# Kernel optimization log

Measured on AMD Instinct MI355X. Metric: run time of the kernel, lower is better.

Reference implementation:

```python
import jax, jax.numpy as jnp
import numpy as np
from jax.scipy.special import logsumexp

N, T, C, H, V = 8, 512, 1024, 256, 32000


def _res_layer(x, W1, b1, W2, b2):
    # hmm-lm ResLayer: x + ReLU(Linear(ReLU(Linear(x))))
    return x + jax.nn.relu(jax.nn.relu(x @ W1.T + b1) @ W2.T + b2)


def setup_inputs() -> dict:
    key = jax.random.key(0)
    ks = jax.random.split(key, 12)
    g = lambda k, shape: jax.random.normal(k, shape, jnp.float32) * (1.0 / np.sqrt(shape[-1]))
    return {
        "text": jax.random.randint(ks[0], (N, T), 0, V),
        "start_emb": jax.random.normal(ks[1], (H,), jnp.float32),
        "start_lin_W": g(ks[2], (H, H)),
        "start_lin_b": jnp.zeros((H,), jnp.float32),
        "start_res_W1": g(ks[3], (2, H, H)),
        "start_res_b1": jnp.zeros((2, H), jnp.float32),
        "start_res_W2": g(ks[4], (2, H, H)),
        "start_res_b2": jnp.zeros((2, H), jnp.float32),
        "state_emb": g(ks[5], (C, H)),
        "next_state_emb": g(ks[6], (C, H)),
        "preterminal_emb": g(ks[7], (C, H)),
        "term_res_W1": g(ks[8], (2, H, H)),
        "term_res_b1": jnp.zeros((2, H), jnp.float32),
        "term_res_W2": g(ks[9], (2, H, H)),
        "term_res_b2": jnp.zeros((2, H), jnp.float32),
        "terminal_emb": g(ks[10], (V, H)),
    }


def reference(text, start_emb, start_lin_W, start_lin_b,
              start_res_W1, start_res_b1, start_res_W2, start_res_b2,
              state_emb, next_state_emb, preterminal_emb,
              term_res_W1, term_res_b1, term_res_W2, term_res_b2,
              terminal_emb):
    # --- start distribution: start_mlp(start_emb) @ next_state_emb.T (tie_start) ---
    fx = start_emb @ start_lin_W.T + start_lin_b
    for i in range(2):
        fx = _res_layer(fx, start_res_W1[i], start_res_b1[i], start_res_W2[i], start_res_b2[i])
    start = jax.nn.log_softmax(fx @ next_state_emb.T)            # [C]

    # --- transition: log_softmax(state_emb @ next_state_emb.T) ---
    transition = jax.nn.log_softmax(state_emb @ next_state_emb.T, axis=-1)  # [C, C]

    # --- emission: log_softmax(terminal_mlp(preterminal_emb) @ terminal_emb.T) ---
    ft = preterminal_emb
    for i in range(2):
        ft = _res_layer(ft, term_res_W1[i], term_res_b1[i], term_res_W2[i], term_res_b2[i])
    emission = jax.nn.log_softmax(ft @ terminal_emb.T, axis=-1)  # [C, V]
    emis_t = emission.T                                          # [V, C]

    # --- HMM forward (log-space) scan; evidence = logsumexp(alpha_T) summed over batch ---
    alpha0 = start[None, :] + emis_t[text[:, 0]]                 # [N, C]

    def step(alpha, x_t):
        # alpha: [N, C]; x_t: [N]
        a = logsumexp(alpha[:, :, None] + transition[None], axis=1) + emis_t[x_t]
        return a, None

    alpha_T, _ = jax.lax.scan(step, alpha0, text[:, 1:].T)       # time-major [T-1, N]
    evidence = logsumexp(alpha_T, axis=-1).sum()
    return evidence
```

## Files before the change

### kernel.cpp

```cpp
#include <hip/hip_runtime.h>
#include <stdint.h>
#include <stddef.h>

#define N_ 8
#define T_ 512
#define C_ 1024
#define H_ 256
#define V_ 32000
#define KC 32
#define CW 32

#define OFF_START   0u
#define OFF_LSE     4096u
#define OFF_EVP     8192u
#define OFF_EA      16384u
#define OFF_FT      81920u
#define OFF_P       1130496u
#define OFF_PART    5324800u
#define OFF_EEXP    5849088u

typedef __attribute__((ext_vector_type(8))) short short8;
typedef __attribute__((ext_vector_type(4))) float floatx4;

__device__ __forceinline__ float dot4(float4 a, float4 b) {
  return a.x*b.x + a.y*b.y + a.z*b.z + a.w*b.w;
}

__device__ __forceinline__ unsigned short f2bf(float f) {
  unsigned u = __float_as_uint(f);
  unsigned r = u + 0x7fffu + ((u >> 16) & 1u);
  return (unsigned short)(r >> 16);
}

__device__ __forceinline__ unsigned pk_bf2(float x, float y) {
  return ((unsigned)f2bf(y) << 16) | (unsigned)f2bf(x);
}

__device__ __forceinline__ short8 pack8(float4 a, float4 b) {
  union { short8 s; unsigned u[4]; } r;
  r.u[0] = pk_bf2(a.x, a.y);
  r.u[1] = pk_bf2(a.z, a.w);
  r.u[2] = pk_bf2(b.x, b.y);
  r.u[3] = pk_bf2(b.z, b.w);
  return r.s;
}

__global__ __launch_bounds__(256) void k_start(
    const float* __restrict__ se, const float* __restrict__ lw, const float* __restrict__ lb,
    const float* __restrict__ W1, const float* __restrict__ b1,
    const float* __restrict__ W2, const float* __restrict__ b2,
    const float* __restrict__ nse, float* __restrict__ out_start)
{
  __shared__ float xs[H_], fx[H_], h1[H_];
  __shared__ float lg[C_];
  __shared__ float redk[4];
  int tid = threadIdx.x;
  xs[tid] = se[tid];
  __syncthreads();
  {
    float acc = lb[tid];
    const float4* wr = (const float4*)(lw + (size_t)tid*H_);
    for (int k = 0; k < H_/4; ++k) acc += dot4(wr[k], *(const float4*)&xs[k*4]);
    fx[tid] = acc;
  }
  __syncthreads();
  for (int L = 0; L < 2; ++L) {
    {
      float acc = b1[L*H_ + tid];
      const float4* wr = (const float4*)(W1 + (size_t)(L*H_ + tid)*H_);
      for (int k = 0; k < H_/4; ++k) acc += dot4(wr[k], *(const float4*)&fx[k*4]);
      h1[tid] = fmaxf(acc, 0.f);
    }
    __syncthreads();
    {
      float acc = b2[L*H_ + tid];
      const float4* wr = (const float4*)(W2 + (size_t)(L*H_ + tid)*H_);
      for (int k = 0; k < H_/4; ++k) acc += dot4(wr[k], *(const float4*)&h1[k*4]);
      fx[tid] += fmaxf(acc, 0.f);
    }
    __syncthreads();
  }
  float lmax = -1e30f;
  for (int r = 0; r < 4; ++r) {
    int cc = tid + r*256;
    float acc = 0.f;
    const float4* er = (const float4*)(nse + (size_t)cc*H_);
    for (int k = 0; k < H_/4; ++k) acc += dot4(er[k], *(const float4*)&fx[k*4]);
    lg[cc] = acc;
    lmax = fmaxf(lmax, acc);
  }
  for (int m = 32; m; m >>= 1) lmax = fmaxf(lmax, __shfl_xor(lmax, m, 64));
  if ((tid & 63) == 0) redk[tid >> 6] = lmax;
  __syncthreads();
  float M = fmaxf(fmaxf(redk[0], redk[1]), fmaxf(redk[2], redk[3]));
  __syncthreads();
  float ssum = 0.f;
  for (int r = 0; r < 4; ++r) ssum += __expf(lg[tid + r*256] - M);
  for (int m = 32; m; m >>= 1) ssum += __shfl_xor(ssum, m, 64);
  if ((tid & 63) == 0) redk[tid >> 6] = ssum;
  __syncthreads();
  float S = redk[0] + redk[1] + redk[2] + redk[3];
  float lse = M + __logf(S);
  for (int r = 0; r < 4; ++r) {
    int cc = tid + r*256;
    out_start[cc] = lg[cc] - lse;
  }
}

__global__ __launch_bounds__(256) void k_gemm_cc(
    const float* __restrict__ A, const float* __restrict__ B, float* __restrict__ Cout)
{
  __shared__ float As[64][69];
  __shared__ float Bs[64][69];
  int tid = threadIdx.x;
  int bi = blockIdx.y, bj = blockIdx.x;
  int sr = tid >> 2, sq = tid & 3;
  int tx = tid & 15, ty = tid >> 4;
  float acc[4][4] = {};
  for (int kb = 0; kb < H_; kb += 64) {
    __syncthreads();
    {
      const float* ar = A + (size_t)(bi*64 + sr)*H_ + kb + sq*16;
      const float* br = B + (size_t)(bj*64 + sr)*H_ + kb + sq*16;
#pragma unroll
      for (int qq = 0; qq < 4; ++qq) {
        float4 av = *(const float4*)(ar + qq*4);
        float4 bv = *(const float4*)(br + qq*4);
        int kk = sq*16 + qq*4;
        As[sr][kk+0]=av.x; As[sr][kk+1]=av.y; As[sr][kk+2]=av.z; As[sr][kk+3]=av.w;
        Bs[sr][kk+0]=bv.x; Bs[sr][kk+1]=bv.y; Bs[sr][kk+2]=bv.z; Bs[sr][kk+3]=bv.w;
      }
    }
    __syncthreads();
#pragma unroll 4
    for (int k = 0; k < 64; ++k) {
      float a0 = As[ty*4+0][k], a1 = As[ty*4+1][k], a2 = As[ty*4+2][k], a3 = As[ty*4+3][k];
      float b0 = Bs[tx*4+0][k], b1 = Bs[tx*4+1][k], b2 = Bs[tx*4+2][k], b3 = Bs[tx*4+3][k];
      acc[0][0]+=a0*b0; acc[0][1]+=a0*b1; acc[0][2]+=a0*b2; acc[0][3]+=a0*b3;
      acc[1][0]+=a1*b0; acc[1][1]+=a1*b1; acc[1][2]+=a1*b2; acc[1][3]+=a1*b3;
      acc[2][0]+=a2*b0; acc[2][1]+=a2*b1; acc[2][2]+=a2*b2; acc[2][3]+=a2*b3;
      acc[3][0]+=a3*b0; acc[3][1]+=a3*b1; acc[3][2]+=a3*b2; acc[3][3]+=a3*b3;
    }
  }
#pragma unroll
  for (int ii = 0; ii < 4; ++ii)
#pragma unroll
    for (int jj = 0; jj < 4; ++jj)
      Cout[(size_t)(bi*64 + ty*4 + ii)*C_ + bj*64 + tx*4 + jj] = acc[ii][jj];
}

__global__ __launch_bounds__(256) void k_softmax_rows(float* __restrict__ P)
{
  __shared__ float redk[4];
  int row = blockIdx.x, tid = threadIdx.x;
  float4* pr = (float4*)(P + (size_t)row*C_);
  float4 v = pr[tid];
  float m = fmaxf(fmaxf(v.x, v.y), fmaxf(v.z, v.w));
  for (int mm = 32; mm; mm >>= 1) m = fmaxf(m, __shfl_xor(m, mm, 64));
  if ((tid & 63) == 0) redk[tid >> 6] = m;
  __syncthreads();
  float M = fmaxf(fmaxf(redk[0], redk[1]), fmaxf(redk[2], redk[3]));
  __syncthreads();
  float4 e;
  e.x = __expf(v.x - M); e.y = __expf(v.y - M); e.z = __expf(v.z - M); e.w = __expf(v.w - M);
  float s = e.x + e.y + e.z + e.w;
  for (int mm = 32; mm; mm >>= 1) s += __shfl_xor(s, mm, 64);
  if ((tid & 63) == 0) redk[tid >> 6] = s;
  __syncthreads();
  float S = redk[0] + redk[1] + redk[2] + redk[3];
  float inv = 1.0f / S;
  e.x *= inv; e.y *= inv; e.z *= inv; e.w *= inv;
  pr[tid] = e;
}

__global__ __launch_bounds__(256) void k_mlp(
    const float* __restrict__ inp, const float* __restrict__ W1, const float* __restrict__ b1,
    const float* __restrict__ W2, const float* __restrict__ b2, float* __restrict__ ft)
{
  __shared__ float xs[4][H_];
  __shared__ float hs[4][H_];
  int tid = threadIdx.x;
  int r0 = blockIdx.x * 4;
  int lr = tid >> 6, lc = (tid & 63) * 4;
  *(float4*)&xs[lr][lc] = *(const float4*)(inp + (size_t)(r0+lr)*H_ + lc);
  __syncthreads();
  for (int L = 0; L < 2; ++L) {
    {
      const float4* wr = (const float4*)(W1 + (size_t)(L*H_ + tid)*H_);
      float bb = b1[L*H_ + tid];
      float a0=bb, a1=bb, a2=bb, a3=bb;
      for (int k = 0; k < H_/4; ++k) {
        float4 w = wr[k];
        a0 += dot4(w, *(const float4*)&xs[0][k*4]);
        a1 += dot4(w, *(const float4*)&xs[1][k*4]);
        a2 += dot4(w, *(const float4*)&xs[2][k*4]);
        a3 += dot4(w, *(const float4*)&xs[3][k*4]);
      }
      hs[0][tid]=fmaxf(a0,0.f); hs[1][tid]=fmaxf(a1,0.f);
      hs[2][tid]=fmaxf(a2,0.f); hs[3][tid]=fmaxf(a3,0.f);
    }
    __syncthreads();
    {
      const float4* wr = (const float4*)(W2 + (size_t)(L*H_ + tid)*H_);
      float bb = b2[L*H_ + tid];
      float a0=bb, a1=bb, a2=bb, a3=bb;
      for (int k = 0; k < H_/4; ++k) {
        float4 w = wr[k];
        a0 += dot4(w, *(const float4*)&hs[0][k*4]);
        a1 += dot4(w, *(const float4*)&hs[1][k*4]);
        a2 += dot4(w, *(const float4*)&hs[2][k*4]);
        a3 += dot4(w, *(const float4*)&hs[3][k*4]);
      }
      xs[0][tid] += fmaxf(a0,0.f); xs[1][tid] += fmaxf(a1,0.f);
      xs[2][tid] += fmaxf(a2,0.f); xs[3][tid] += fmaxf(a3,0.f);
    }
    __syncthreads();
  }
  *(float4*)(ft + (size_t)(r0+lr)*H_ + lc) = *(float4*)&xs[lr][lc];
}

#define LSE_VSPLIT 16
#define LSE_VPB    2000
#define LSE_CHUNKS 125

__global__ __launch_bounds__(256) void k_lse_mfma(
    const float* __restrict__ ft, const float* __restrict__ emb, float* __restrict__ part)
{
  int tid = threadIdx.x;
  int lane = tid & 63;
  int w = tid >> 6;
  int q = blockIdx.x;
  int jb = blockIdx.y * 64 + w * 16;
  int r16 = lane & 15, kb = lane >> 4;

  short8 A[8];
  {
    const float* arow = ft + (size_t)(jb + r16) * H_ + kb * 8;
#pragma unroll
    for (int ks = 0; ks < 8; ++ks) {
      float4 a = *(const float4*)(arow + ks * 32);
      float4 b = *(const float4*)(arow + ks * 32 + 4);
      A[ks] = pack8(a, b);
    }
  }
  float s0 = 0.f, s1 = 0.f, s2 = 0.f, s3 = 0.f;
  const float* embq = emb + (size_t)q * LSE_VPB * H_;
#pragma unroll 1
  for (int ch = 0; ch < LSE_CHUNKS; ++ch) {
    const float* brow = embq + (size_t)(ch * 16 + r16) * H_ + kb * 8;
    floatx4 acca = {0,0,0,0}, accb = {0,0,0,0};
#pragma unroll
    for (int ks = 0; ks < 8; ks += 2) {
      float4 x0 = *(const float4*)(brow + ks * 32);
      float4 y0 = *(const float4*)(brow + ks * 32 + 4);
      float4 x1 = *(const float4*)(brow + ks * 32 + 32);
      float4 y1 = *(const float4*)(brow + ks * 32 + 36);
      acca = __builtin_amdgcn_mfma_f32_16x16x32_bf16(A[ks],   pack8(x0, y0), acca, 0, 0, 0);
      accb = __builtin_amdgcn_mfma_f32_16x16x32_bf16(A[ks+1], pack8(x1, y1), accb, 0, 0, 0);
    }
    s0 += __expf(acca[0] + accb[0]);
    s1 += __expf(acca[1] + accb[1]);
    s2 += __expf(acca[2] + accb[2]);
    s3 += __expf(acca[3] + accb[3]);
  }
#pragma unroll
  for (int mm = 1; mm <= 8; mm <<= 1) {
    s0 += __shfl_xor(s0, mm, 64);
    s1 += __shfl_xor(s1, mm, 64);
    s2 += __shfl_xor(s2, mm, 64);
    s3 += __shfl_xor(s3, mm, 64);
  }
  if (r16 == 0) {
    int jrow = jb + kb * 4;
    part[(size_t)(jrow + 0) * LSE_VSPLIT + q] = s0;
    part[(size_t)(jrow + 1) * LSE_VSPLIT + q] = s1;
    part[(size_t)(jrow + 2) * LSE_VSPLIT + q] = s2;
    part[(size_t)(jrow + 3) * LSE_VSPLIT + q] = s3;
  }
}

__global__ __launch_bounds__(256) void k_lse_reduce(
    const float* __restrict__ part, float* __restrict__ lse_row)
{
  int row = blockIdx.x * 256 + threadIdx.x;
  const float4* p = (const float4*)(part + (size_t)row * LSE_VSPLIT);
  float4 a = p[0], b = p[1], c = p[2], d = p[3];
  float s = a.x+a.y+a.z+a.w + b.x+b.y+b.z+b.w + c.x+c.y+c.z+c.w + d.x+d.y+d.z+d.w;
  lse_row[row] = __logf(s);
}

__global__ __launch_bounds__(256) void k_eexp_mfma(
    const float* __restrict__ ft, const float* __restrict__ emb, const int* __restrict__ text,
    const float* __restrict__ lse_row, float* __restrict__ EEXP)
{
  int tid = threadIdx.x;
  int lane = tid & 63;
  int w = tid >> 6;
  int jb = blockIdx.y * 64 + w * 16;
  int tb = blockIdx.x * 64;
  int r16 = lane & 15, kb = lane >> 4;

  short8 A[8];
  {
    const float* arow = ft + (size_t)(jb + r16) * H_ + kb * 8;
#pragma unroll
    for (int ks = 0; ks < 8; ++ks) {
      float4 a = *(const float4*)(arow + ks * 32);
      float4 b = *(const float4*)(arow + ks * 32 + 4);
      A[ks] = pack8(a, b);
    }
  }
  float4 lsej = *(const float4*)(lse_row + jb + kb * 4);

#pragma unroll 1
  for (int tc = 0; tc < 4; ++tc) {
    int idx = tb + tc * 16 + r16;
    int tok = text[idx];
    const float* brow = emb + (size_t)tok * H_ + kb * 8;
    floatx4 acca = {0,0,0,0}, accb = {0,0,0,0};
#pragma unroll
    for (int ks = 0; ks < 8; ks += 2) {
      float4 x0 = *(const float4*)(brow + ks * 32);
      float4 y0 = *(const float4*)(brow + ks * 32 + 4);
      float4 x1 = *(const float4*)(brow + ks * 32 + 32);
      float4 y1 = *(const float4*)(brow + ks * 32 + 36);
      acca = __builtin_amdgcn_mfma_f32_16x16x32_bf16(A[ks],   pack8(x0, y0), acca, 0, 0, 0);
      accb = __builtin_amdgcn_mfma_f32_16x16x32_bf16(A[ks+1], pack8(x1, y1), accb, 0, 0, 0);
    }
    float4 o;
    o.x = __expf(acca[0] + accb[0] - lsej.x);
    o.y = __expf(acca[1] + accb[1] - lsej.y);
    o.z = __expf(acca[2] + accb[2] - lsej.z);
    o.w = __expf(acca[3] + accb[3] - lsej.w);
    *(float4*)(EEXP + (size_t)idx * C_ + jb + kb * 4) = o;
  }
}

#define SCAN_LDS 75792

#define BF_ACC(PU, RI) { \
    float plo_ = __uint_as_float((PU) << 16); \
    float phi_ = __uint_as_float((PU) & 0xffff0000u); \
    acc[jo][0] += plo_ * ea0[(RI)];   acc[jo][0] += phi_ * ea0[(RI)+1]; \
    acc[jo][1] += plo_ * ea1[(RI)];   acc[jo][1] += phi_ * ea1[(RI)+1]; }

__global__ __launch_bounds__(256) void k_scan(
    const float* __restrict__ P, const float* __restrict__ EEXP, const float* __restrict__ startv,
    unsigned* __restrict__ eaG, float* __restrict__ evp)
{
  extern __shared__ char smem[];
  char*  Pl  = smem;
  float* eal = (float*)(smem + 65536);
  float* red = (float*)(smem + 65536 + 9216);
  float* gmw = (float*)(smem + 65536 + 9216 + 1024);

  int tid = threadIdx.x;
  int bid = blockIdx.x;
  int c  = bid >> 2;
  int ng = bid & 3;
  int n0 = ng * 2;

  if (tid < 64) {
    int nn = tid >> 5, j = tid & 31;
    int jj = c*CW + j;
    float val = __expf(startv[jj]) * EEXP[((size_t)(n0+nn)*T_ + 0)*C_ + jj];
    unsigned word = ((unsigned)f2bf(val) << 16) | 1u;
    __hip_atomic_store(&eaG[(size_t)(0*N_ + n0+nn)*C_ + jj], word,
                       __ATOMIC_RELAXED, __HIP_MEMORY_SCOPE_AGENT);
  }

  {
    int j4  = (tid & 7) * 4;
    int swz = (tid & 7) << 4;
    int irow = tid >> 3;
    for (int rep = 0; rep < 32; ++rep) {
      int i = rep*32 + irow;
      float4 v = *(const float4*)(P + (size_t)i*C_ + c*CW + j4);
      int ib = (i*2) ^ swz;
      *(unsigned short*)(Pl + (j4+0)*2048 + ib) = f2bf(v.x);
      *(unsigned short*)(Pl + (j4+1)*2048 + ib) = f2bf(v.y);
      *(unsigned short*)(Pl + (j4+2)*2048 + ib) = f2bf(v.z);
      *(unsigned short*)(Pl + (j4+3)*2048 + ib) = f2bf(v.w);
    }
  }
  __syncthreads();

  float logscale0 = 0.f, logscale1 = 0.f;

#pragma unroll 1
  for (int t = 1; t < T_; ++t) {
    int pprev = (t-1) & 1, pcur = t & 1;

    float eexp_reg = 0.f;
    if (tid < 64) {
      int nn = tid >> 5, j = tid & 31;
      eexp_reg = EEXP[((size_t)(n0+nn)*T_ + t)*C_ + c*CW + j];
    }

    {
      int seq = tid >> 7;
      int ib  = (tid & 127) * 8;
      unsigned long long* src = (unsigned long long*)(eaG + ((size_t)(pprev*N_ + n0+seq)*C_ + ib));
      unsigned tgt = (unsigned)t;
      unsigned long long v0, v1, v2, v3;
      int guard = 0;
      for (;;) {
        v0 = __hip_atomic_load(src+0, __ATOMIC_RELAXED, __HIP_MEMORY_SCOPE_AGENT);
        v1 = __hip_atomic_load(src+1, __ATOMIC_RELAXED, __HIP_MEMORY_SCOPE_AGENT);
        v2 = __hip_atomic_load(src+2, __ATOMIC_RELAXED, __HIP_MEMORY_SCOPE_AGENT);
        v3 = __hip_atomic_load(src+3, __ATOMIC_RELAXED, __HIP_MEMORY_SCOPE_AGENT);
        bool ok = (((unsigned)v0 & 0xffffu) == tgt) & (((unsigned)(v0>>32) & 0xffffu) == tgt)
                & (((unsigned)v1 & 0xffffu) == tgt) & (((unsigned)(v1>>32) & 0xffffu) == tgt)
                & (((unsigned)v2 & 0xffffu) == tgt) & (((unsigned)(v2>>32) & 0xffffu) == tgt)
                & (((unsigned)v3 & 0xffffu) == tgt) & (((unsigned)(v3>>32) & 0xffffu) == tgt);
        if (ok) break;
        __builtin_amdgcn_s_sleep(1);
        if (++guard > 2000000) break;
      }
      float f0 = __uint_as_float((unsigned)v0        & 0xffff0000u);
      float f1 = __uint_as_float((unsigned)(v0>>32)  & 0xffff0000u);
      float f2 = __uint_as_float((unsigned)v1        & 0xffff0000u);
      float f3 = __uint_as_float((unsigned)(v1>>32)  & 0xffff0000u);
      float f4v= __uint_as_float((unsigned)v2        & 0xffff0000u);
      float f5 = __uint_as_float((unsigned)(v2>>32)  & 0xffff0000u);
      float f6 = __uint_as_float((unsigned)v3        & 0xffff0000u);
      float f7 = __uint_as_float((unsigned)(v3>>32)  & 0xffff0000u);
      int idx = ib + ((ib >> 5) << 2);
      float* dst = &eal[seq*1152 + idx];
      dst[0]=f0; dst[1]=f1; dst[2]=f2; dst[3]=f3;
      dst[4]=f4v; dst[5]=f5; dst[6]=f6; dst[7]=f7;
      float m8 = fmaxf(fmaxf(fmaxf(f0,f1),fmaxf(f2,f3)), fmaxf(fmaxf(f4v,f5),fmaxf(f6,f7)));
#pragma unroll
      for (int mm = 32; mm; mm >>= 1) m8 = fmaxf(m8, __shfl_xor(m8, mm, 64));
      if ((tid & 63) == 0) gmw[tid >> 6] = m8;
    }
    __syncthreads();

    float M0 = fmaxf(gmw[0], gmw[1]);
    float M1 = fmaxf(gmw[2], gmw[3]);
    logscale0 += __logf(M0);
    logscale1 += __logf(M1);

    float ea0[32], ea1[32];
    {
      int s = tid >> 3;
      int eb = s * 36;
#pragma unroll
      for (int w = 0; w < 8; ++w) {
        float4 a = *(const float4*)&eal[eb + w*4];
        float4 b = *(const float4*)&eal[1152 + eb + w*4];
        ea0[w*4+0]=a.x; ea0[w*4+1]=a.y; ea0[w*4+2]=a.z; ea0[w*4+3]=a.w;
        ea1[w*4+0]=b.x; ea1[w*4+1]=b.y; ea1[w*4+2]=b.z; ea1[w*4+3]=b.w;
      }
    }
    float acc[4][2] = {{0,0},{0,0},{0,0},{0,0}};
    {
      int g = tid & 7, s = tid >> 3;
      int i0b = s * 64;
      int swz = g << 4;
#pragma unroll
      for (int jo = 0; jo < 4; ++jo) {
        const char* bp = Pl + (size_t)(g*4 + jo)*2048;
#pragma unroll
        for (int u = 0; u < 4; ++u) {
          uint4 pk = *(const uint4*)(bp + ((i0b + u*16) ^ swz));
          BF_ACC(pk.x, u*8+0)
          BF_ACC(pk.y, u*8+2)
          BF_ACC(pk.z, u*8+4)
          BF_ACC(pk.w, u*8+6)
        }
      }
    }
#pragma unroll
    for (int jo = 0; jo < 4; ++jo)
#pragma unroll
      for (int nn = 0; nn < 2; ++nn) {
        float vv = acc[jo][nn];
        vv += __shfl_xor(vv, 8, 64);
        vv += __shfl_xor(vv, 16, 64);
        vv += __shfl_xor(vv, 32, 64);
        acc[jo][nn] = vv;
      }
    if ((tid & 63) < 8) {
      int wv = tid >> 6, g = tid & 7;
#pragma unroll
      for (int jo = 0; jo < 4; ++jo) {
        red[((wv*8 + g)*4 + jo)*2 + 0] = acc[jo][0];
        red[((wv*8 + g)*4 + jo)*2 + 1] = acc[jo][1];
      }
    }
    __syncthreads();
    if (tid < 64) {
      int nn = tid >> 5, j = tid & 31;
      int gg = j >> 2, joo = j & 3;
      float sum = red[((0*8+gg)*4+joo)*2+nn] + red[((1*8+gg)*4+joo)*2+nn]
                + red[((2*8+gg)*4+joo)*2+nn] + red[((3*8+gg)*4+joo)*2+nn];
      float M = (nn == 0) ? M0 : M1;
      float val = (sum / M) * eexp_reg;
      unsigned word = ((unsigned)f2bf(val) << 16) | (unsigned)(t+1);
      __hip_atomic_store(&eaG[(size_t)(pcur*N_ + n0+nn)*C_ + c*CW + j], word,
                         __ATOMIC_RELAXED, __HIP_MEMORY_SCOPE_AGENT);
    }
  }

  if (c == 0) {
    {
      int seq = tid >> 7;
      int ib  = (tid & 127) * 8;
      unsigned long long* src = (unsigned long long*)(eaG + ((size_t)(1*N_ + n0+seq)*C_ + ib));
      unsigned tgt = (unsigned)T_;
      unsigned long long v0, v1, v2, v3;
      int guard = 0;
      for (;;) {
        v0 = __hip_atomic_load(src+0, __ATOMIC_RELAXED, __HIP_MEMORY_SCOPE_AGENT);
        v1 = __hip_atomic_load(src+1, __ATOMIC_RELAXED, __HIP_MEMORY_SCOPE_AGENT);
        v2 = __hip_atomic_load(src+2, __ATOMIC_RELAXED, __HIP_MEMORY_SCOPE_AGENT);
        v3 = __hip_atomic_load(src+3, __ATOMIC_RELAXED, __HIP_MEMORY_SCOPE_AGENT);
        bool ok = (((unsigned)v0 & 0xffffu) == tgt) & (((unsigned)(v0>>32) & 0xffffu) == tgt)
                & (((unsigned)v1 & 0xffffu) == tgt) & (((unsigned)(v1>>32) & 0xffffu) == tgt)
                & (((unsigned)v2 & 0xffffu) == tgt) & (((unsigned)(v2>>32) & 0xffffu) == tgt)
                & (((unsigned)v3 & 0xffffu) == tgt) & (((unsigned)(v3>>32) & 0xffffu) == tgt);
        if (ok) break;
        __builtin_amdgcn_s_sleep(1);
        if (++guard > 2000000) break;
      }
      float s8 = __uint_as_float((unsigned)v0       & 0xffff0000u)
               + __uint_as_float((unsigned)(v0>>32) & 0xffff0000u)
               + __uint_as_float((unsigned)v1       & 0xffff0000u)
               + __uint_as_float((unsigned)(v1>>32) & 0xffff0000u)
               + __uint_as_float((unsigned)v2       & 0xffff0000u)
               + __uint_as_float((unsigned)(v2>>32) & 0xffff0000u)
               + __uint_as_float((unsigned)v3       & 0xffff0000u)
               + __uint_as_float((unsigned)(v3>>32) & 0xffff0000u);
#pragma unroll
      for (int mm = 32; mm; mm >>= 1) s8 += __shfl_xor(s8, mm, 64);
      if ((tid & 63) == 0) gmw[tid >> 6] = s8;
    }
    __syncthreads();
    if (tid == 0) {
      float S0 = gmw[0] + gmw[1];
      float S1 = gmw[2] + gmw[3];
      evp[n0]     = logscale0 + __logf(S0);
      evp[n0 + 1] = logscale1 + __logf(S1);
    }
  }
}

__global__ void k_final(const float* __restrict__ evp, float* __restrict__ out)
{
  if (threadIdx.x == 0) {
    float s = 0.f;
#pragma unroll
    for (int i = 0; i < N_; ++i) s += evp[i];
    out[0] = s;
  }
}

extern "C" void kernel_launch(void* const* d_in, const int* in_sizes, int n_in,
                              void* d_out, int out_size, void* d_ws, size_t ws_size,
                              hipStream_t stream)
{
  const int*   text      = (const int*)  d_in[0];
  const float* start_emb = (const float*)d_in[1];
  const float* slw       = (const float*)d_in[2];
  const float* slb       = (const float*)d_in[3];
  const float* sW1       = (const float*)d_in[4];
  const float* sb1       = (const float*)d_in[5];
  const float* sW2       = (const float*)d_in[6];
  const float* sb2       = (const float*)d_in[7];
  const float* state_emb = (const float*)d_in[8];
  const float* nse       = (const float*)d_in[9];
  const float* pre_emb   = (const float*)d_in[10];
  const float* tW1       = (const float*)d_in[11];
  const float* tb1       = (const float*)d_in[12];
  const float* tW2       = (const float*)d_in[13];
  const float* tb2       = (const float*)d_in[14];
  const float* term_emb  = (const float*)d_in[15];

  char* ws = (char*)d_ws;
  float*    w_start = (float*)   (ws + OFF_START);
  float*    w_lse   = (float*)   (ws + OFF_LSE);
  float*    w_evp   = (float*)   (ws + OFF_EVP);
  unsigned* w_ea    = (unsigned*)(ws + OFF_EA);
  float*    w_ft    = (float*)   (ws + OFF_FT);
  float*    w_P     = (float*)   (ws + OFF_P);
  float*    w_part  = (float*)   (ws + OFF_PART);
  float*    w_eexp  = (float*)   (ws + OFF_EEXP);

  (void)hipMemsetAsync(w_ea, 0, 2*N_*C_*sizeof(unsigned), stream);

  k_start<<<1, 256, 0, stream>>>(start_emb, slw, slb, sW1, sb1, sW2, sb2, nse, w_start);
  k_gemm_cc<<<dim3(16,16), 256, 0, stream>>>(state_emb, nse, w_P);
  k_softmax_rows<<<C_, 256, 0, stream>>>(w_P);
  k_mlp<<<C_/4, 256, 0, stream>>>(pre_emb, tW1, tb1, tW2, tb2, w_ft);
  k_lse_mfma<<<dim3(LSE_VSPLIT, 16), 256, 0, stream>>>(w_ft, term_emb, w_part);
  k_lse_reduce<<<4, 256, 0, stream>>>(w_part, w_lse);
  k_eexp_mfma<<<dim3(64, 16), 256, 0, stream>>>(w_ft, term_emb, text, w_lse, w_eexp);

  (void)hipFuncSetAttribute((const void*)k_scan, hipFuncAttributeMaxDynamicSharedMemorySize, SCAN_LDS);
  k_scan<<<128, 256, SCAN_LDS, stream>>>(w_P, w_eexp, w_start, w_ea, w_evp);
  k_final<<<1, 64, 0, stream>>>(w_evp, (float*)d_out);
}
```

Measured before the change: 1.941 ms.

## Scan all 8 sequences per block with MFMA bf16 matvec over 32 blocks

The forward scan now runs on 32 blocks, each handling all 8 sequences for a 32-column slice, in place of 128 blocks each handling 2 sequences. The per-step matrix-vector product becomes a bf16 MFMA of an 8x1024 alpha tile against the LDS-resident transition slice, replacing scalar FMAs. This cuts the number of blocks that poll the global flag words each step and reuses each P slice across all sequences. In exchange each block does more work per step, with fewer CUs involved and wider polling loads per thread.

After: 2.554 ms. 1.32x slower.

```diff
diff --git a/kernel.cpp b/kernel.cpp
--- a/kernel.cpp
+++ b/kernel.cpp
@@ -7,7 +7,6 @@
 #define C_ 1024
 #define H_ 256
 #define V_ 32000
-#define KC 32
 #define CW 32
 
 #define OFF_START   0u
@@ -336,13 +335,7 @@
   }
 }
 
-#define SCAN_LDS 75792
-
-#define BF_ACC(PU, RI) { \
-    float plo_ = __uint_as_float((PU) << 16); \
-    float phi_ = __uint_as_float((PU) & 0xffff0000u); \
-    acc[jo][0] += plo_ * ea0[(RI)];   acc[jo][0] += phi_ * ea0[(RI)+1]; \
-    acc[jo][1] += plo_ * ea1[(RI)];   acc[jo][1] += phi_ * ea1[(RI)+1]; }
+#define SCAN_LDS (65536 + 16384 + 4096 + 32)
 
 __global__ __launch_bounds__(256) void k_scan(
     const float* __restrict__ P, const float* __restrict__ EEXP, const float* __restrict__ startv,
@@ -350,199 +343,163 @@
 {
   extern __shared__ char smem[];
   char*  Pl  = smem;
-  float* eal = (float*)(smem + 65536);
-  float* red = (float*)(smem + 65536 + 9216);
-  float* gmw = (float*)(smem + 65536 + 9216 + 1024);
-
-  int tid = threadIdx.x;
-  int bid = blockIdx.x;
-  int c  = bid >> 2;
-  int ng = bid & 3;
-  int n0 = ng * 2;
-
-  if (tid < 64) {
-    int nn = tid >> 5, j = tid & 31;
-    int jj = c*CW + j;
-    float val = __expf(startv[jj]) * EEXP[((size_t)(n0+nn)*T_ + 0)*C_ + jj];
+  char*  Al  = smem + 65536;
+  float* red = (float*)(smem + 65536 + 16384);
+  float* gmw = (float*)(smem + 65536 + 16384 + 4096);
+
+  int tid  = threadIdx.x;
+  int c    = blockIdx.x;
+  int lane = tid & 63;
+  int w    = tid >> 6;
+  int seq  = tid >> 5;
+  int jj   = tid & 31;
+
+  {
+    int col = c*CW + jj;
+    float val = __expf(startv[col]) * EEXP[((size_t)seq*T_ + 0)*C_ + col];
     unsigned word = ((unsigned)f2bf(val) << 16) | 1u;
-    __hip_atomic_store(&eaG[(size_t)(0*N_ + n0+nn)*C_ + jj], word,
+    __hip_atomic_store(&eaG[(size_t)(0*N_ + seq)*C_ + col], word,
                        __ATOMIC_RELAXED, __HIP_MEMORY_SCOPE_AGENT);
   }
 
   {
-    int j4  = (tid & 7) * 4;
-    int swz = (tid & 7) << 4;
+    int j4 = (tid & 7) * 4;
     int irow = tid >> 3;
     for (int rep = 0; rep < 32; ++rep) {
       int i = rep*32 + irow;
       float4 v = *(const float4*)(P + (size_t)i*C_ + c*CW + j4);
-      int ib = (i*2) ^ swz;
-      *(unsigned short*)(Pl + (j4+0)*2048 + ib) = f2bf(v.x);
-      *(unsigned short*)(Pl + (j4+1)*2048 + ib) = f2bf(v.y);
-      *(unsigned short*)(Pl + (j4+2)*2048 + ib) = f2bf(v.z);
-      *(unsigned short*)(Pl + (j4+3)*2048 + ib) = f2bf(v.w);
-    }
-  }
-  __syncthreads();
-
-  float logscale0 = 0.f, logscale1 = 0.f;
+      int ib = 2*i;
+      *(unsigned short*)(Pl + (size_t)(j4+0)*2048 + (ib ^ (((j4+0)&7)<<4))) = f2bf(v.x);
+      *(unsigned short*)(Pl + (size_t)(j4+1)*2048 + (ib ^ (((j4+1)&7)<<4))) = f2bf(v.y);
+      *(unsigned short*)(Pl + (size_t)(j4+2)*2048 + (ib ^ (((j4+2)&7)<<4))) = f2bf(v.z);
+      *(unsigned short*)(Pl + (size_t)(j4+3)*2048 + (ib ^ (((j4+3)&7)<<4))) = f2bf(v.w);
+    }
+  }
+  __syncthreads();
+
+  float logscale = 0.f;
+  const unsigned long long TMASK = 0x0000ffff0000ffffULL;
 
 #pragma unroll 1
   for (int t = 1; t < T_; ++t) {
     int pprev = (t-1) & 1, pcur = t & 1;
 
-    float eexp_reg = 0.f;
-    if (tid < 64) {
-      int nn = tid >> 5, j = tid & 31;
-      eexp_reg = EEXP[((size_t)(n0+nn)*T_ + t)*C_ + c*CW + j];
-    }
-
-    {
-      int seq = tid >> 7;
-      int ib  = (tid & 127) * 8;
-      unsigned long long* src = (unsigned long long*)(eaG + ((size_t)(pprev*N_ + n0+seq)*C_ + ib));
-      unsigned tgt = (unsigned)t;
-      unsigned long long v0, v1, v2, v3;
+    float eexp_reg = EEXP[((size_t)seq*T_ + t)*C_ + c*CW + jj];
+
+    {
+      int k0 = jj * 32;
+      unsigned long long* src = (unsigned long long*)(eaG + ((size_t)(pprev*N_ + seq)*C_ + k0));
+      unsigned long long tpair = (unsigned long long)(unsigned)t | ((unsigned long long)(unsigned)t << 32);
+      unsigned long long v[16];
       int guard = 0;
       for (;;) {
-        v0 = __hip_atomic_load(src+0, __ATOMIC_RELAXED, __HIP_MEMORY_SCOPE_AGENT);
-        v1 = __hip_atomic_load(src+1, __ATOMIC_RELAXED, __HIP_MEMORY_SCOPE_AGENT);
-        v2 = __hip_atomic_load(src+2, __ATOMIC_RELAXED, __HIP_MEMORY_SCOPE_AGENT);
-        v3 = __hip_atomic_load(src+3, __ATOMIC_RELAXED, __HIP_MEMORY_SCOPE_AGENT);
-        bool ok = (((unsigned)v0 & 0xffffu) == tgt) & (((unsigned)(v0>>32) & 0xffffu) == tgt)
-                & (((unsigned)v1 & 0xffffu) == tgt) & (((unsigned)(v1>>32) & 0xffffu) == tgt)
-                & (((unsigned)v2 & 0xffffu) == tgt) & (((unsigned)(v2>>32) & 0xffffu) == tgt)
-                & (((unsigned)v3 & 0xffffu) == tgt) & (((unsigned)(v3>>32) & 0xffffu) == tgt);
+#pragma unroll
+        for (int u = 0; u < 16; ++u)
+          v[u] = __hip_atomic_load(src+u, __ATOMIC_RELAXED, __HIP_MEMORY_SCOPE_AGENT);
+        bool ok = true;
+#pragma unroll
+        for (int u = 0; u < 16; ++u) ok &= ((v[u] & TMASK) == tpair);
         if (ok) break;
         __builtin_amdgcn_s_sleep(1);
         if (++guard > 2000000) break;
       }
-      float f0 = __uint_as_float((unsigned)v0        & 0xffff0000u);
-      float f1 = __uint_as_float((unsigned)(v0>>32)  & 0xffff0000u);
-      float f2 = __uint_as_float((unsigned)v1        & 0xffff0000u);
-      float f3 = __uint_as_float((unsigned)(v1>>32)  & 0xffff0000u);
-      float f4v= __uint_as_float((unsigned)v2        & 0xffff0000u);
-      float f5 = __uint_as_float((unsigned)(v2>>32)  & 0xffff0000u);
-      float f6 = __uint_as_float((unsigned)v3        & 0xffff0000u);
-      float f7 = __uint_as_float((unsigned)(v3>>32)  & 0xffff0000u);
-      int idx = ib + ((ib >> 5) << 2);
-      float* dst = &eal[seq*1152 + idx];
-      dst[0]=f0; dst[1]=f1; dst[2]=f2; dst[3]=f3;
-      dst[4]=f4v; dst[5]=f5; dst[6]=f6; dst[7]=f7;
-      float m8 = fmaxf(fmaxf(fmaxf(f0,f1),fmaxf(f2,f3)), fmaxf(fmaxf(f4v,f5),fmaxf(f6,f7)));
-#pragma unroll
-      for (int mm = 32; mm; mm >>= 1) m8 = fmaxf(m8, __shfl_xor(m8, mm, 64));
-      if ((tid & 63) == 0) gmw[tid >> 6] = m8;
-    }
-    __syncthreads();
-
-    float M0 = fmaxf(gmw[0], gmw[1]);
-    float M1 = fmaxf(gmw[2], gmw[3]);
-    logscale0 += __logf(M0);
-    logscale1 += __logf(M1);
-
-    float ea0[32], ea1[32];
-    {
-      int s = tid >> 3;
-      int eb = s * 36;
-#pragma unroll
-      for (int w = 0; w < 8; ++w) {
-        float4 a = *(const float4*)&eal[eb + w*4];
-        float4 b = *(const float4*)&eal[1152 + eb + w*4];
-        ea0[w*4+0]=a.x; ea0[w*4+1]=a.y; ea0[w*4+2]=a.z; ea0[w*4+3]=a.w;
-        ea1[w*4+0]=b.x; ea1[w*4+1]=b.y; ea1[w*4+2]=b.z; ea1[w*4+3]=b.w;
-      }
-    }
-    float acc[4][2] = {{0,0},{0,0},{0,0},{0,0}};
-    {
-      int g = tid & 7, s = tid >> 3;
-      int i0b = s * 64;
-      int swz = g << 4;
-#pragma unroll
-      for (int jo = 0; jo < 4; ++jo) {
-        const char* bp = Pl + (size_t)(g*4 + jo)*2048;
-#pragma unroll
-        for (int u = 0; u < 4; ++u) {
-          uint4 pk = *(const uint4*)(bp + ((i0b + u*16) ^ swz));
-          BF_ACC(pk.x, u*8+0)
-          BF_ACC(pk.y, u*8+2)
-          BF_ACC(pk.z, u*8+4)
-          BF_ACC(pk.w, u*8+6)
-        }
-      }
-    }
-#pragma unroll
-    for (int jo = 0; jo < 4; ++jo)
-#pragma unroll
-      for (int nn = 0; nn < 2; ++nn) {
-        float vv = acc[jo][nn];
-        vv += __shfl_xor(vv, 8, 64);
-        vv += __shfl_xor(vv, 16, 64);
-        vv += __shfl_xor(vv, 32, 64);
-        acc[jo][nn] = vv;
-      }
-    if ((tid & 63) < 8) {
-      int wv = tid >> 6, g = tid & 7;
-#pragma unroll
-      for (int jo = 0; jo < 4; ++jo) {
-        red[((wv*8 + g)*4 + jo)*2 + 0] = acc[jo][0];
-        red[((wv*8 + g)*4 + jo)*2 + 1] = acc[jo][1];
-      }
-    }
-    __syncthreads();
-    if (tid < 64) {
-      int nn = tid >> 5, j = tid & 31;
-      int gg = j >> 2, joo = j & 3;
-      float sum = red[((0*8+gg)*4+joo)*2+nn] + red[((1*8+gg)*4+joo)*2+nn]
-                + red[((2*8+gg)*4+joo)*2+nn] + red[((3*8+gg)*4+joo)*2+nn];
-      float M = (nn == 0) ? M0 : M1;
-      float val = (sum / M) * eexp_reg;
+      float m = 0.f;
+      unsigned pk[16];
+#pragma unroll
+      for (int u = 0; u < 16; ++u) {
+        unsigned wlo = (unsigned)v[u], whi = (unsigned)(v[u] >> 32);
+        m = fmaxf(m, fmaxf(__uint_as_float(wlo & 0xffff0000u),
+                           __uint_as_float(whi & 0xffff0000u)));
+        pk[u] = (wlo >> 16) | (whi & 0xffff0000u);
+      }
+      char* dst = Al + seq*2048;
+      int kb2 = 2*k0;
+#pragma unroll
+      for (int q = 0; q < 4; ++q)
+        *(uint4*)(dst + ((kb2 + q*16) ^ (seq<<4))) = *(const uint4*)&pk[q*4];
+#pragma unroll
+      for (int mm = 16; mm; mm >>= 1) m = fmaxf(m, __shfl_xor(m, mm, 64));
+      if (jj == 0) gmw[seq] = m;
+    }
+    __syncthreads();
+
+    if (tid < 8) logscale += __logf(gmw[tid]);
+
+    short8 Afrag[8];
+    {
+      int r = lane & 7;
+      int ks = (lane >> 4) * 8;
+      char* ap = Al + (size_t)r*2048;
+      int rswz = r << 4;
+#pragma unroll
+      for (int kb = 0; kb < 8; ++kb) {
+        int kby = 2*(w*256 + kb*32 + ks);
+        Afrag[kb] = *(const short8*)(ap + (kby ^ rswz));
+      }
+    }
+    int j0 = lane & 15;
+    const char* bp0 = Pl + (size_t)j0*2048;
+    const char* bp1 = Pl + (size_t)(16+j0)*2048;
+    int jswz = (j0 & 7) << 4;
+    int ks = (lane >> 4) * 8;
+    floatx4 acc0 = {0,0,0,0}, acc1 = {0,0,0,0};
+#pragma unroll
+    for (int kb = 0; kb < 8; ++kb) {
+      int kby = 2*(w*256 + kb*32 + ks);
+      short8 b0 = *(const short8*)(bp0 + (kby ^ jswz));
+      short8 b1 = *(const short8*)(bp1 + (kby ^ jswz));
+      acc0 = __builtin_amdgcn_mfma_f32_16x16x32_bf16(Afrag[kb], b0, acc0, 0, 0, 0);
+      acc1 = __builtin_amdgcn_mfma_f32_16x16x32_bf16(Afrag[kb], b1, acc1, 0, 0, 0);
+    }
+    if (lane < 32) {
+      int rbase = (lane >> 4) * 4;
+#pragma unroll
+      for (int q = 0; q < 4; ++q) {
+        red[((w*2+0)*8 + rbase + q)*16 + j0] = acc0[q];
+        red[((w*2+1)*8 + rbase + q)*16 + j0] = acc1[q];
+      }
+    }
+    __syncthreads();
+
+    {
+      int tb = jj >> 4, jc = jj & 15;
+      float sum = red[((0*2+tb)*8 + seq)*16 + jc] + red[((1*2+tb)*8 + seq)*16 + jc]
+                + red[((2*2+tb)*8 + seq)*16 + jc] + red[((3*2+tb)*8 + seq)*16 + jc];
+      float val = (sum / gmw[seq]) * eexp_reg;
       unsigned word = ((unsigned)f2bf(val) << 16) | (unsigned)(t+1);
-      __hip_atomic_store(&eaG[(size_t)(pcur*N_ + n0+nn)*C_ + c*CW + j], word,
+      __hip_atomic_store(&eaG[(size_t)(pcur*N_ + seq)*C_ + c*CW + jj], word,
                          __ATOMIC_RELAXED, __HIP_MEMORY_SCOPE_AGENT);
     }
   }
 
   if (c == 0) {
-    {
-      int seq = tid >> 7;
-      int ib  = (tid & 127) * 8;
-      unsigned long long* src = (unsigned long long*)(eaG + ((size_t)(1*N_ + n0+seq)*C_ + ib));
-      unsigned tgt = (unsigned)T_;
-      unsigned long long v0, v1, v2, v3;
-      int guard = 0;
-      for (;;) {
-        v0 = __hip_atomic_load(src+0, __ATOMIC_RELAXED, __HIP_MEMORY_SCOPE_AGENT);
-        v1 = __hip_atomic_load(src+1, __ATOMIC_RELAXED, __HIP_MEMORY_SCOPE_AGENT);
-        v2 = __hip_atomic_load(src+2, __ATOMIC_RELAXED, __HIP_MEMORY_SCOPE_AGENT);
-        v3 = __hip_atomic_load(src+3, __ATOMIC_RELAXED, __HIP_MEMORY_SCOPE_AGENT);
-        bool ok = (((unsigned)v0 & 0xffffu) == tgt) & (((unsigned)(v0>>32) & 0xffffu) == tgt)
-                & (((unsigned)v1 & 0xffffu) == tgt) & (((unsigned)(v1>>32) & 0xffffu) == tgt)
-                & (((unsigned)v2 & 0xffffu) == tgt) & (((unsigned)(v2>>32) & 0xffffu) == tgt)
-                & (((unsigned)v3 & 0xffffu) == tgt) & (((unsigned)(v3>>32) & 0xffffu) == tgt);
-        if (ok) break;
-        __builtin_amdgcn_s_sleep(1);
-        if (++guard > 2000000) break;
-      }
-      float s8 = __uint_as_float((unsigned)v0       & 0xffff0000u)
-               + __uint_as_float((unsigned)(v0>>32) & 0xffff0000u)
-               + __uint_as_float((unsigned)v1       & 0xffff0000u)
-               + __uint_as_float((unsigned)(v1>>32) & 0xffff0000u)
-               + __uint_as_float((unsigned)v2       & 0xffff0000u)
-               + __uint_as_float((unsigned)(v2>>32) & 0xffff0000u)
-               + __uint_as_float((unsigned)v3       & 0xffff0000u)
-               + __uint_as_float((unsigned)(v3>>32) & 0xffff0000u);
-#pragma unroll
-      for (int mm = 32; mm; mm >>= 1) s8 += __shfl_xor(s8, mm, 64);
-      if ((tid & 63) == 0) gmw[tid >> 6] = s8;
-    }
-    __syncthreads();
-    if (tid == 0) {
-      float S0 = gmw[0] + gmw[1];
-      float S1 = gmw[2] + gmw[3];
-      evp[n0]     = logscale0 + __logf(S0);
-      evp[n0 + 1] = logscale1 + __logf(S1);
-    }
+    int k0 = jj * 32;
+    unsigned long long* src = (unsigned long long*)(eaG + ((size_t)(1*N_ + seq)*C_ + k0));
+    unsigned long long tpair = (unsigned long long)(unsigned)T_ | ((unsigned long long)(unsigned)T_ << 32);
+    unsigned long long v[16];
+    int guard = 0;
+    for (;;) {
+#pragma unroll
+      for (int u = 0; u < 16; ++u)
+        v[u] = __hip_atomic_load(src+u, __ATOMIC_RELAXED, __HIP_MEMORY_SCOPE_AGENT);
+      bool ok = true;
+#pragma unroll
+      for (int u = 0; u < 16; ++u) ok &= ((v[u] & TMASK) == tpair);
+      if (ok) break;
+      __builtin_amdgcn_s_sleep(1);
+      if (++guard > 2000000) break;
+    }
+    float s8 = 0.f;
+#pragma unroll
+    for (int u = 0; u < 16; ++u) {
+      s8 += __uint_as_float((unsigned)v[u]        & 0xffff0000u);
+      s8 += __uint_as_float((unsigned)(v[u]>>32)  & 0xffff0000u);
+    }
+#pragma unroll
+    for (int mm = 16; mm; mm >>= 1) s8 += __shfl_xor(s8, mm, 64);
+    if (jj == 0) gmw[seq] = s8;
+    __syncthreads();
+    if (tid < 8) evp[tid] = logscale + __logf(gmw[tid]);
   }
 }
 
@@ -598,6 +555,6 @@
   k_eexp_mfma<<<dim3(64, 16), 256, 0, stream>>>(w_ft, term_emb, text, w_lse, w_eexp);
 
   (void)hipFuncSetAttribute((const void*)k_scan, hipFuncAttributeMaxDynamicSharedMemorySize, SCAN_LDS);
-  k_scan<<<128, 256, SCAN_LDS, stream>>>(w_P, w_eexp, w_start, w_ea, w_evp);
+  k_scan<<<32, 256, SCAN_LDS, stream>>>(w_P, w_eexp, w_start, w_ea, w_evp);
   k_final<<<1, 64, 0, stream>>>(w_evp, (float*)d_out);
 }
```
